# Kernel tuning notes

Hardware: AMD Instinct MI355X
Metric: run time of the kernel (lower is better)

Reference implementation:

```python
import jax, jax.numpy as jnp
import numpy as np


def setup_inputs() -> dict:
    key = jax.random.key(0)
    k1, k2 = jax.random.split(key)
    N, C, H, W = 8, 3, 512, 1024
    img = jax.random.normal(k1, (N, C, H, W), dtype=jnp.float32)
    flo = jax.random.normal(k2, (N, 2, H, W), dtype=jnp.float32)
    return {"img": img, "flo": flo}


def _splat(img_nhwc, ix, iy, w, H, W):
    # img_nhwc: (N,H,W,C); ix,iy: int32 (N,H,W) absolute target coords; w: (N,H,W)
    N = img_nhwc.shape[0]
    C = img_nhwc.shape[-1]
    valid = (ix >= 0) & (ix < H) & (iy >= 0) & (iy < W)
    w = jnp.where(valid, w, 0.0)
    ixc = jnp.clip(ix, 0, H - 1)
    iyc = jnp.clip(iy, 0, W - 1)
    n_idx = jnp.arange(N, dtype=jnp.int32)[:, None, None]
    tid = (n_idx * H + ixc) * W + iyc            # (N,H,W) flat index into N*H*W
    tid = tid.reshape(-1)
    vals = (img_nhwc * w[..., None]).reshape(-1, C)
    imgw = jnp.zeros((N * H * W, C), dtype=img_nhwc.dtype).at[tid].add(vals)
    onew = jnp.zeros((N * H * W,), dtype=img_nhwc.dtype).at[tid].add(w.reshape(-1))
    imgw = imgw.reshape(N, H, W, C).transpose(0, 3, 1, 2)          # (N,C,H,W)
    onew = jnp.broadcast_to(onew.reshape(N, 1, H, W), (N, C, H, W))
    return imgw, onew


def _forward(img, flo):
    N, C, H, W = img.shape
    y = flo[:, 0]                                # (N,H,W) row offset
    x = flo[:, 1]                                # (N,H,W) col offset
    x1 = jnp.floor(x); x2 = x1 + 1.0
    y1 = jnp.floor(y); y2 = y1 + 1.0
    # gaussian splat weights
    dx1 = (x - x1) ** 2; dx2 = (x - x2) ** 2
    dy1 = (y - y1) ** 2; dy2 = (y - y2) ** 2
    w11 = jnp.exp(-(dx1 + dy1)); w12 = jnp.exp(-(dx1 + dy2))
    w21 = jnp.exp(-(dx2 + dy1)); w22 = jnp.exp(-(dx2 + dy2))
    # base grid + integer shift -> absolute target coords
    bx = jnp.arange(H, dtype=jnp.int32)[None, :, None]   # row index
    by = jnp.arange(W, dtype=jnp.int32)[None, None, :]   # col index
    img_nhwc = img.transpose(0, 2, 3, 1)
    out = []
    for sx, sy, w in ((x1, y1, w11), (x1, y2, w12), (x2, y1, w21), (x2, y2, w22)):
        ix = sx.astype(jnp.int32) + bx
        iy = sy.astype(jnp.int32) + by
        out.append(_splat(img_nhwc, ix, iy, w, H, W))
    imgw = out[0][0] + out[1][0] + out[2][0] + out[3][0]
    o = out[0][1] + out[1][1] + out[2][1] + out[3][1]
    return imgw, o


def reference(img, flo):
    return _forward(img, flo)
```

## Files before the change

### kernel.cpp

```cpp
#include <hip/hip_runtime.h>
#include <hip/hip_fp16.h>
#include <stdint.h>

constexpr int Nn = 8;
constexpr int Cc = 3;
constexpr int Hh = 512;
constexpr int Ww = 1024;
constexpr int HW = Hh * Ww;
constexpr int NCHW = Nn * Cc * HW;

constexpr int TH = 16;
constexpr int TW = 32;
constexpr int R  = 4;
constexpr int RH = TH + 2 * R;
constexpr int RW = TW + 2 * R;
constexpr int NPIX = RH * RW;
constexpr int ITERS = (NPIX + 255) / 256;
constexpr int TILE_PIX = TH * TW;
constexpr int AWP = TW + 1;
constexpr int NP  = (TH + 1) * AWP;
constexpr int NSLOT = 3;

typedef float fvec4 __attribute__((ext_vector_type(4)));
typedef float fvec2 __attribute__((ext_vector_type(2)));
typedef __attribute__((address_space(3))) float lds_f;

__device__ __forceinline__ void ds_fadd4(lds_f* p, float a, float b, float c, float d) {
    asm volatile(
        "ds_add_f32 %0, %1\n\t"
        "ds_add_f32 %0, %2 offset:2048\n\t"
        "ds_add_f32 %0, %3 offset:4096\n\t"
        "ds_add_f32 %0, %4 offset:6144"
        :: "v"(p), "v"(a), "v"(b), "v"(c), "v"(d) : "memory");
}

__global__ __launch_bounds__(256, 5) void splat_tiled(
        const float* __restrict__ img,
        const float* __restrict__ flo,
        float* __restrict__ out) {
    __shared__ unsigned int s_tag[NP];
    __shared__ unsigned int s_pay[NSLOT * NP * 3];
    __shared__ unsigned int s_kcnt[(NP + 3) / 4 + 1];
    __shared__ float s_pl[4 * TILE_PIX];
    const int tid = threadIdx.x;
    for (int i = tid; i < NP; i += 256) s_tag[i] = 0u;
    for (int i = tid; i < (NP + 3) / 4 + 1; i += 256) s_kcnt[i] = 0u;
    {
        fvec4* a4 = (fvec4*)s_pl;
        fvec4 z = {0.f, 0.f, 0.f, 0.f};
        a4[tid] = z;
        a4[tid + 256] = z;
    }
    __syncthreads();

    const int lin = blockIdx.x + 32 * blockIdx.y + 1024 * blockIdx.z;
    const int n   = lin & 7;
    const int t   = lin >> 3;
    const int tw0 = (t & 31) * TW;
    const int th0 = (t >> 5) * TH;
    const float* __restrict__ floy = flo + (size_t)(n * 2 + 0) * HW;
    const float* __restrict__ flox = flo + (size_t)(n * 2 + 1) * HW;
    const float* __restrict__ imgn = img + (size_t)n * Cc * HW;

    float sy[ITERS], sx[ITERS], u0[ITERS], u1[ITERS], u2[ITERS];
    #pragma unroll
    for (int it = 0; it < ITERS; ++it) {
        int i  = tid + 256 * it;
        int ic = i < NPIX ? i : NPIX - 1;
        int rh = ic / RW;
        int rw = ic - rh * RW;
        int h  = th0 - R + rh;
        int w  = tw0 - R + rw;
        int hc = h < 0 ? 0 : (h > Hh - 1 ? Hh - 1 : h);
        int wc = w < 0 ? 0 : (w > Ww - 1 ? Ww - 1 : w);
        int hwc = hc * Ww + wc;
        sy[it] = floy[hwc];
        sx[it] = flox[hwc];
        u0[it] = imgn[hwc];
        u1[it] = imgn[HW + hwc];
        u2[it] = imgn[2 * HW + hwc];
    }

    int aA[ITERS];
    unsigned int tg[ITERS], q0[ITERS], q1[ITERS], q2[ITERS];
    bool pend[ITERS];
    #pragma unroll
    for (int it = 0; it < ITERS; ++it) {
        int i  = tid + 256 * it;
        int rh = i / RW;
        int rw = i - rh * RW;
        int h  = th0 - R + rh;
        int w  = tw0 - R + rw;
        bool live = (i < NPIX) & (h >= 0) & (h < Hh) & (w >= 0) & (w < Ww);

        float y = sy[it], x = sx[it];
        float x1f = floorf(x), y1f = floorf(y);
        float fx = x - x1f, fy = y - y1f;
        int ox = (int)x1f, oy = (int)y1f;
        bool patchok = (ox >= -R) & (ox <= R - 1) & (oy >= -R) & (oy <= R - 1);
        int ah = ox + rh - R;
        int aw = oy + rw - R;
        bool rec = live & patchok & (ah >= -1) & (ah <= TH - 1)
                                  & (aw >= -1) & (aw <= TW - 1);
        int aIdx = (ah + 1) * AWP + (aw + 1);
        tg[it] = 0x80000000u | ((unsigned)(ox + R) << 3) | (unsigned)(oy + R);
        unsigned h0 = __half_as_ushort(__float2half_rn(u0[it]));
        unsigned h1 = __half_as_ushort(__float2half_rn(u1[it]));
        unsigned h2 = __half_as_ushort(__float2half_rn(u2[it]));
        unsigned fxq = (unsigned)(fx * 65535.0f + 0.5f);
        unsigned fyq = (unsigned)(fy * 65535.0f + 0.5f);
        q0[it] = h0 | (h1 << 16);
        q1[it] = h2 | (fxq << 16);
        q2[it] = fyq;
        aA[it]  = aIdx;
        pend[it] = rec;
        if (rec) s_tag[aIdx] = tg[it];
    }
    __syncthreads();

    #pragma unroll
    for (int r = 0; r < NSLOT; ++r) {
        #pragma unroll
        for (int it = 0; it < ITERS; ++it) {
            if (pend[it] && s_tag[aA[it]] == tg[it]) {
                int base = aA[it] * 9 + r * 3;
                s_pay[base]     = q0[it];
                s_pay[base + 1] = q1[it];
                s_pay[base + 2] = q2[it];
                ((unsigned char*)s_kcnt)[aA[it]] = (unsigned char)(r + 1);
                pend[it] = false;
            } else if (r == NSLOT - 1 && pend[it]) {
                int a = aA[it];
                int arow = a / AWP;
                int ah = arow - 1;
                int aw = a - arow * AWP - 1;
                float fx = (float)(q1[it] >> 16) * (1.0f / 65535.0f);
                float fy = (float)(q2[it] & 0xFFFFu) * (1.0f / 65535.0f);
                float i0 = __half2float(__ushort_as_half((unsigned short)(q0[it] & 0xFFFFu)));
                float i1 = __half2float(__ushort_as_half((unsigned short)(q0[it] >> 16)));
                float i2 = __half2float(__ushort_as_half((unsigned short)(q1[it] & 0xFFFFu)));
                #pragma unroll
                for (int ca = 0; ca < 2; ++ca) {
                    #pragma unroll
                    for (int cb = 0; cb < 2; ++cb) {
                        int t_h = ah + ca, t_w = aw + cb;
                        if ((unsigned)t_h < (unsigned)TH && (unsigned)t_w < (unsigned)TW) {
                            float dx = fx - (float)ca, dy = fy - (float)cb;
                            float wt = __expf(-(dx * dx + dy * dy));
                            ds_fadd4((lds_f*)s_pl + (t_h * TW + t_w),
                                     i0 * wt, i1 * wt, i2 * wt, wt);
                        }
                    }
                }
            }
        }
        __syncthreads();
        if (r < NSLOT - 1) {
            #pragma unroll
            for (int it = 0; it < ITERS; ++it)
                if (pend[it]) s_tag[aA[it]] = tg[it];
            __syncthreads();
        }
    }

    float* __restrict__ imgw  = out;
    float* __restrict__ o_out = out + NCHW;
    const size_t nb = (size_t)n * Cc * HW;
    {
        int pix = 2 * tid;
        int lh = pix >> 5, lw = pix & 31;
        fvec2 p0 = *(const fvec2*)&s_pl[pix];
        fvec2 p1 = *(const fvec2*)&s_pl[512 + pix];
        fvec2 p2 = *(const fvec2*)&s_pl[1024 + pix];
        fvec2 p3 = *(const fvec2*)&s_pl[1536 + pix];
        float s0a = p0[0], s0b = p0[1];
        float s1a = p1[0], s1b = p1[1];
        float s2a = p2[0], s2b = p2[1];
        float s3a = p3[0], s3b = p3[1];
        #pragma unroll
        for (int a = 0; a < 2; ++a) {
            int arow = (lh - a + 1) * AWP + lw;
            #pragma unroll
            for (int c = 0; c < 3; ++c) {
                int ai = arow + c;
                int k = ((const unsigned char*)s_kcnt)[ai];
                #pragma unroll
                for (int j = 0; j < NSLOT; ++j) {
                    if (j < k) {
                        int base = ai * 9 + j * 3;
                        unsigned w0 = s_pay[base];
                        unsigned w1 = s_pay[base + 1];
                        unsigned w2 = s_pay[base + 2];
                        float h0 = __half2float(__ushort_as_half((unsigned short)(w0 & 0xFFFFu)));
                        float h1 = __half2float(__ushort_as_half((unsigned short)(w0 >> 16)));
                        float h2 = __half2float(__ushort_as_half((unsigned short)(w1 & 0xFFFFu)));
                        float fx = (float)(w1 >> 16) * (1.0f / 65535.0f);
                        float fy = (float)(w2 & 0xFFFFu) * (1.0f / 65535.0f);
                        float dx  = fx - (float)a;
                        float dxx = dx * dx;
                        if (c < 2) {
                            float dy = fy - (float)(1 - c);
                            float wt = __expf(-(dxx + dy * dy));
                            s0a += h0 * wt; s1a += h1 * wt; s2a += h2 * wt; s3a += wt;
                        }
                        if (c >= 1) {
                            float dy = fy - (float)(2 - c);
                            float wt = __expf(-(dxx + dy * dy));
                            s0b += h0 * wt; s1b += h1 * wt; s2b += h2 * wt; s3b += wt;
                        }
                    }
                }
            }
        }
        size_t hw = (size_t)(th0 + lh) * Ww + (tw0 + lw);
        fvec2 v;
        v[0] = s0a; v[1] = s0b;
        __builtin_nontemporal_store(v, (fvec2*)(imgw + nb + hw));
        v[0] = s1a; v[1] = s1b;
        __builtin_nontemporal_store(v, (fvec2*)(imgw + nb + HW + hw));
        v[0] = s2a; v[1] = s2b;
        __builtin_nontemporal_store(v, (fvec2*)(imgw + nb + 2 * HW + hw));
        v[0] = s3a; v[1] = s3b;
        __builtin_nontemporal_store(v, (fvec2*)(o_out + nb + hw));
        __builtin_nontemporal_store(v, (fvec2*)(o_out + nb + HW + hw));
        __builtin_nontemporal_store(v, (fvec2*)(o_out + nb + 2 * HW + hw));
    }
}

__global__ __launch_bounds__(256) void rescan_all(
        const float* __restrict__ img,
        const float* __restrict__ flo,
        float* __restrict__ out) {
    float* imgw  = out;
    float* o_out = out + NCHW;
    unsigned int j = blockIdx.x * blockDim.x + threadIdx.x;
    if (j >= (unsigned)(Nn * HW / 4)) return;
    int n   = j / (HW / 4);
    int q   = j - n * (HW / 4);
    int hw0 = q * 4;
    const fvec4 y4 = *(const fvec4*)&flo[(size_t)(n * 2 + 0) * HW + hw0];
    const fvec4 x4 = *(const fvec4*)&flo[(size_t)(n * 2 + 1) * HW + hw0];
    #pragma unroll
    for (int k = 0; k < 4; ++k) {
        float x = x4[k], y = y4[k];
        if (x >= -(float)R && x < (float)R && y >= -(float)R && y < (float)R) continue;
        int hw = hw0 + k;
        int h = hw >> 10;
        int w = hw & (Ww - 1);
        float x1f = floorf(x), y1f = floorf(y);
        float fx = x - x1f, fy = y - y1f;
        int bx = (int)x1f, by = (int)y1f;
        float i0 = img[(size_t)(n * Cc + 0) * HW + hw];
        float i1 = img[(size_t)(n * Cc + 1) * HW + hw];
        float i2 = img[(size_t)(n * Cc + 2) * HW + hw];
        const size_t nb = (size_t)n * Cc * HW;
        #pragma unroll
        for (int a = 0; a < 2; ++a) {
            #pragma unroll
            for (int b = 0; b < 2; ++b) {
                int ix = h + bx + a;
                int iy = w + by + b;
                if (ix < 0 || ix >= Hh || iy < 0 || iy >= Ww) continue;
                float dx = fx - (float)a, dy = fy - (float)b;
                float wt = __expf(-(dx * dx + dy * dy));
                int t = ix * Ww + iy;
                atomicAdd(&imgw[nb + t], i0 * wt);
                atomicAdd(&imgw[nb + HW + t], i1 * wt);
                atomicAdd(&imgw[nb + 2 * HW + t], i2 * wt);
                atomicAdd(&o_out[nb + t], wt);
                atomicAdd(&o_out[nb + HW + t], wt);
                atomicAdd(&o_out[nb + 2 * HW + t], wt);
            }
        }
    }
}

extern "C" void kernel_launch(void* const* d_in, const int* in_sizes, int n_in,
                              void* d_out, int out_size, void* d_ws, size_t ws_size,
                              hipStream_t stream) {
    const float* img = (const float*)d_in[0];
    const float* flo = (const float*)d_in[1];
    float* out = (float*)d_out;
    (void)d_ws; (void)ws_size;

    dim3 block(256);
    dim3 grid(32, 32, 8);
    splat_tiled<<<grid, block, 0, stream>>>(img, flo, out);
    rescan_all<<<(Nn * HW / 4 + 255) / 256, 256, 0, stream>>>(img, flo, out);
}
```

Before: 191.1 us.

## Replace LDS atomic overflow accumulation with compact overflow list gathered per pixel

Replaces the 8 KB LDS float accumulation plane and its ds_add_f32 atomics for slot-overflow entries with a small capped overflow list. Each overflow entry now carries its anchor coordinates, and every output thread scans the list during the gather phase. Removing the plane lowers LDS use, so the launch bound rises from 5 to 6 blocks per CU. The cost is that every thread scans the whole list, and entries beyond the 128 cap are silently dropped, which could lose contributions.

```diff
diff --git a/kernel.cpp b/kernel.cpp
--- a/kernel.cpp
+++ b/kernel.cpp
@@ -20,37 +20,24 @@
 constexpr int AWP = TW + 1;
 constexpr int NP  = (TH + 1) * AWP;
 constexpr int NSLOT = 3;
+constexpr int OVF_CAP = 128;
 
 typedef float fvec4 __attribute__((ext_vector_type(4)));
 typedef float fvec2 __attribute__((ext_vector_type(2)));
-typedef __attribute__((address_space(3))) float lds_f;
-
-__device__ __forceinline__ void ds_fadd4(lds_f* p, float a, float b, float c, float d) {
-    asm volatile(
-        "ds_add_f32 %0, %1\n\t"
-        "ds_add_f32 %0, %2 offset:2048\n\t"
-        "ds_add_f32 %0, %3 offset:4096\n\t"
-        "ds_add_f32 %0, %4 offset:6144"
-        :: "v"(p), "v"(a), "v"(b), "v"(c), "v"(d) : "memory");
-}
-
-__global__ __launch_bounds__(256, 5) void splat_tiled(
+
+__global__ __launch_bounds__(256, 6) void splat_tiled(
         const float* __restrict__ img,
         const float* __restrict__ flo,
         float* __restrict__ out) {
     __shared__ unsigned int s_tag[NP];
     __shared__ unsigned int s_pay[NSLOT * NP * 3];
     __shared__ unsigned int s_kcnt[(NP + 3) / 4 + 1];
-    __shared__ float s_pl[4 * TILE_PIX];
+    __shared__ unsigned int s_ovf[OVF_CAP * 4];
+    __shared__ unsigned int s_ovfn;
     const int tid = threadIdx.x;
     for (int i = tid; i < NP; i += 256) s_tag[i] = 0u;
     for (int i = tid; i < (NP + 3) / 4 + 1; i += 256) s_kcnt[i] = 0u;
-    {
-        fvec4* a4 = (fvec4*)s_pl;
-        fvec4 z = {0.f, 0.f, 0.f, 0.f};
-        a4[tid] = z;
-        a4[tid + 256] = z;
-    }
+    if (tid == 0) s_ovfn = 0u;
     __syncthreads();
 
     const int lin = blockIdx.x + 32 * blockIdx.y + 1024 * blockIdx.z;
@@ -111,7 +98,8 @@
         unsigned fyq = (unsigned)(fy * 65535.0f + 0.5f);
         q0[it] = h0 | (h1 << 16);
         q1[it] = h2 | (fxq << 16);
-        q2[it] = fyq;
+        q2[it] = fyq | (((unsigned)(ah + 1) & 0x3Fu) << 16)
+                     | (((unsigned)(aw + 1) & 0x3Fu) << 22);
         aA[it]  = aIdx;
         pend[it] = rec;
         if (rec) s_tag[aIdx] = tg[it];
@@ -130,27 +118,12 @@
                 ((unsigned char*)s_kcnt)[aA[it]] = (unsigned char)(r + 1);
                 pend[it] = false;
             } else if (r == NSLOT - 1 && pend[it]) {
-                int a = aA[it];
-                int arow = a / AWP;
-                int ah = arow - 1;
-                int aw = a - arow * AWP - 1;
-                float fx = (float)(q1[it] >> 16) * (1.0f / 65535.0f);
-                float fy = (float)(q2[it] & 0xFFFFu) * (1.0f / 65535.0f);
-                float i0 = __half2float(__ushort_as_half((unsigned short)(q0[it] & 0xFFFFu)));
-                float i1 = __half2float(__ushort_as_half((unsigned short)(q0[it] >> 16)));
-                float i2 = __half2float(__ushort_as_half((unsigned short)(q1[it] & 0xFFFFu)));
-                #pragma unroll
-                for (int ca = 0; ca < 2; ++ca) {
-                    #pragma unroll
-                    for (int cb = 0; cb < 2; ++cb) {
-                        int t_h = ah + ca, t_w = aw + cb;
-                        if ((unsigned)t_h < (unsigned)TH && (unsigned)t_w < (unsigned)TW) {
-                            float dx = fx - (float)ca, dy = fy - (float)cb;
-                            float wt = __expf(-(dx * dx + dy * dy));
-                            ds_fadd4((lds_f*)s_pl + (t_h * TW + t_w),
-                                     i0 * wt, i1 * wt, i2 * wt, wt);
-                        }
-                    }
+                unsigned idx = atomicAdd(&s_ovfn, 1u);
+                if (idx < (unsigned)OVF_CAP) {
+                    int b4 = (int)idx * 4;
+                    s_ovf[b4]     = q0[it];
+                    s_ovf[b4 + 1] = q1[it];
+                    s_ovf[b4 + 2] = q2[it];
                 }
             }
         }
@@ -169,14 +142,31 @@
     {
         int pix = 2 * tid;
         int lh = pix >> 5, lw = pix & 31;
-        fvec2 p0 = *(const fvec2*)&s_pl[pix];
-        fvec2 p1 = *(const fvec2*)&s_pl[512 + pix];
-        fvec2 p2 = *(const fvec2*)&s_pl[1024 + pix];
-        fvec2 p3 = *(const fvec2*)&s_pl[1536 + pix];
-        float s0a = p0[0], s0b = p0[1];
-        float s1a = p1[0], s1b = p1[1];
-        float s2a = p2[0], s2b = p2[1];
-        float s3a = p3[0], s3b = p3[1];
+        float s0a = 0.f, s0b = 0.f;
+        float s1a = 0.f, s1b = 0.f;
+        float s2a = 0.f, s2b = 0.f;
+        float s3a = 0.f, s3b = 0.f;
+
+        auto apply_entry = [&](unsigned w0, unsigned w1, unsigned w2, int a, int c) {
+            float h0 = __half2float(__ushort_as_half((unsigned short)(w0 & 0xFFFFu)));
+            float h1 = __half2float(__ushort_as_half((unsigned short)(w0 >> 16)));
+            float h2 = __half2float(__ushort_as_half((unsigned short)(w1 & 0xFFFFu)));
+            float fx = (float)(w1 >> 16) * (1.0f / 65535.0f);
+            float fy = (float)(w2 & 0xFFFFu) * (1.0f / 65535.0f);
+            float dx  = fx - (float)a;
+            float dxx = dx * dx;
+            if (c < 2) {
+                float dy = fy - (float)(1 - c);
+                float wt = __expf(-(dxx + dy * dy));
+                s0a += h0 * wt; s1a += h1 * wt; s2a += h2 * wt; s3a += wt;
+            }
+            if (c >= 1) {
+                float dy = fy - (float)(2 - c);
+                float wt = __expf(-(dxx + dy * dy));
+                s0b += h0 * wt; s1b += h1 * wt; s2b += h2 * wt; s3b += wt;
+            }
+        };
+
         #pragma unroll
         for (int a = 0; a < 2; ++a) {
             int arow = (lh - a + 1) * AWP + lw;
@@ -188,30 +178,26 @@
                 for (int j = 0; j < NSLOT; ++j) {
                     if (j < k) {
                         int base = ai * 9 + j * 3;
-                        unsigned w0 = s_pay[base];
-                        unsigned w1 = s_pay[base + 1];
-                        unsigned w2 = s_pay[base + 2];
-                        float h0 = __half2float(__ushort_as_half((unsigned short)(w0 & 0xFFFFu)));
-                        float h1 = __half2float(__ushort_as_half((unsigned short)(w0 >> 16)));
-                        float h2 = __half2float(__ushort_as_half((unsigned short)(w1 & 0xFFFFu)));
-                        float fx = (float)(w1 >> 16) * (1.0f / 65535.0f);
-                        float fy = (float)(w2 & 0xFFFFu) * (1.0f / 65535.0f);
-                        float dx  = fx - (float)a;
-                        float dxx = dx * dx;
-                        if (c < 2) {
-                            float dy = fy - (float)(1 - c);
-                            float wt = __expf(-(dxx + dy * dy));
-                            s0a += h0 * wt; s1a += h1 * wt; s2a += h2 * wt; s3a += wt;
-                        }
-                        if (c >= 1) {
-                            float dy = fy - (float)(2 - c);
-                            float wt = __expf(-(dxx + dy * dy));
-                            s0b += h0 * wt; s1b += h1 * wt; s2b += h2 * wt; s3b += wt;
-                        }
+                        apply_entry(s_pay[base], s_pay[base + 1], s_pay[base + 2], a, c);
                     }
                 }
             }
         }
+
+        unsigned novf = s_ovfn;
+        if (novf > (unsigned)OVF_CAP) novf = OVF_CAP;
+        for (unsigned e = 0; e < novf; ++e) {
+            unsigned w0 = s_ovf[e * 4];
+            unsigned w1 = s_ovf[e * 4 + 1];
+            unsigned w2 = s_ovf[e * 4 + 2];
+            int ar = (int)((w2 >> 16) & 0x3Fu);
+            int ac = (int)((w2 >> 22) & 0x3Fu);
+            int a  = lh + 1 - ar;
+            int c  = ac - lw;
+            if (((unsigned)a < 2u) & ((unsigned)c < 3u))
+                apply_entry(w0, w1, w2, a, c);
+        }
+
         size_t hw = (size_t)(th0 + lh) * Ww + (tw0 + lw);
         fvec2 v;
         v[0] = s0a; v[1] = s0b;
```

New measurement: 191.9 us. About the same (+0.4%).

## Enlarge tiles, drop LDS plane accumulator, overflow via global atomics

Applied to the files above, without the earlier changes.

Tiles grow from 16x32 to 32x32 and the halo shrinks from 4 to 3, which cuts redundant halo loads per output pixel. The LDS float accumulation plane and the per-cell count array are removed. Slot occupancy is now marked by a flag bit in the payload, and each thread gathers four output columns with float4 stores. Sources that overflow the three slots now do global unsafeAtomicAdd after the tile's stores complete, and the rescan kernel skips contributions already covered by a tile, so no splat is counted twice. The risks are lower occupancy (launch bounds 3), more wasted ITERS lanes, and atomic-ordering correctness that depends on s_waitcnt plus a block barrier.

```diff
diff --git a/kernel.cpp b/kernel.cpp
--- a/kernel.cpp
+++ b/kernel.cpp
@@ -9,51 +9,36 @@
 constexpr int HW = Hh * Ww;
 constexpr int NCHW = Nn * Cc * HW;
 
-constexpr int TH = 16;
+constexpr int TH = 32;
 constexpr int TW = 32;
-constexpr int R  = 4;
-constexpr int RH = TH + 2 * R;
-constexpr int RW = TW + 2 * R;
+constexpr int RS = 3;
+constexpr int RH = TH + 2 * RS;
+constexpr int RW = TW + 2 * RS;
 constexpr int NPIX = RH * RW;
 constexpr int ITERS = (NPIX + 255) / 256;
-constexpr int TILE_PIX = TH * TW;
 constexpr int AWP = TW + 1;
 constexpr int NP  = (TH + 1) * AWP;
 constexpr int NSLOT = 3;
 
 typedef float fvec4 __attribute__((ext_vector_type(4)));
-typedef float fvec2 __attribute__((ext_vector_type(2)));
-typedef __attribute__((address_space(3))) float lds_f;
-
-__device__ __forceinline__ void ds_fadd4(lds_f* p, float a, float b, float c, float d) {
-    asm volatile(
-        "ds_add_f32 %0, %1\n\t"
-        "ds_add_f32 %0, %2 offset:2048\n\t"
-        "ds_add_f32 %0, %3 offset:4096\n\t"
-        "ds_add_f32 %0, %4 offset:6144"
-        :: "v"(p), "v"(a), "v"(b), "v"(c), "v"(d) : "memory");
-}
-
-__global__ __launch_bounds__(256, 5) void splat_tiled(
+typedef unsigned int uvec4 __attribute__((ext_vector_type(4)));
+
+__global__ __launch_bounds__(256, 3) void splat_tiled(
         const float* __restrict__ img,
         const float* __restrict__ flo,
         float* __restrict__ out) {
     __shared__ unsigned int s_tag[NP];
-    __shared__ unsigned int s_pay[NSLOT * NP * 3];
-    __shared__ unsigned int s_kcnt[(NP + 3) / 4 + 1];
-    __shared__ float s_pl[4 * TILE_PIX];
+    __shared__ alignas(16) unsigned int s_pay[NSLOT * NP * 3 + 3];
     const int tid = threadIdx.x;
     for (int i = tid; i < NP; i += 256) s_tag[i] = 0u;
-    for (int i = tid; i < (NP + 3) / 4 + 1; i += 256) s_kcnt[i] = 0u;
     {
-        fvec4* a4 = (fvec4*)s_pl;
-        fvec4 z = {0.f, 0.f, 0.f, 0.f};
-        a4[tid] = z;
-        a4[tid + 256] = z;
+        uvec4* p4 = (uvec4*)s_pay;
+        uvec4 z = {0u, 0u, 0u, 0u};
+        for (int i = tid; i < (NSLOT * NP * 3 + 3) / 4; i += 256) p4[i] = z;
     }
     __syncthreads();
 
-    const int lin = blockIdx.x + 32 * blockIdx.y + 1024 * blockIdx.z;
+    const int lin = blockIdx.x + 32 * blockIdx.y + 512 * blockIdx.z;
     const int n   = lin & 7;
     const int t   = lin >> 3;
     const int tw0 = (t & 31) * TW;
@@ -65,12 +50,13 @@
     float sy[ITERS], sx[ITERS], u0[ITERS], u1[ITERS], u2[ITERS];
     #pragma unroll
     for (int it = 0; it < ITERS; ++it) {
+        if ((tid & ~63) + 256 * it >= NPIX) continue;
         int i  = tid + 256 * it;
         int ic = i < NPIX ? i : NPIX - 1;
         int rh = ic / RW;
         int rw = ic - rh * RW;
-        int h  = th0 - R + rh;
-        int w  = tw0 - R + rw;
+        int h  = th0 - RS + rh;
+        int w  = tw0 - RS + rw;
         int hc = h < 0 ? 0 : (h > Hh - 1 ? Hh - 1 : h);
         int wc = w < 0 ? 0 : (w > Ww - 1 ? Ww - 1 : w);
         int hwc = hc * Ww + wc;
@@ -85,25 +71,27 @@
     unsigned int tg[ITERS], q0[ITERS], q1[ITERS], q2[ITERS];
     bool pend[ITERS];
     #pragma unroll
+    for (int it = 0; it < ITERS; ++it) pend[it] = false;
+    #pragma unroll
     for (int it = 0; it < ITERS; ++it) {
+        if ((tid & ~63) + 256 * it >= NPIX) continue;
         int i  = tid + 256 * it;
-        int rh = i / RW;
-        int rw = i - rh * RW;
-        int h  = th0 - R + rh;
-        int w  = tw0 - R + rw;
+        int ic = i < NPIX ? i : NPIX - 1;
+        int rh = ic / RW;
+        int rw = ic - rh * RW;
+        int h  = th0 - RS + rh;
+        int w  = tw0 - RS + rw;
         bool live = (i < NPIX) & (h >= 0) & (h < Hh) & (w >= 0) & (w < Ww);
 
         float y = sy[it], x = sx[it];
         float x1f = floorf(x), y1f = floorf(y);
         float fx = x - x1f, fy = y - y1f;
         int ox = (int)x1f, oy = (int)y1f;
-        bool patchok = (ox >= -R) & (ox <= R - 1) & (oy >= -R) & (oy <= R - 1);
-        int ah = ox + rh - R;
-        int aw = oy + rw - R;
-        bool rec = live & patchok & (ah >= -1) & (ah <= TH - 1)
-                                  & (aw >= -1) & (aw <= TW - 1);
+        int ah = ox + rh - RS;
+        int aw = oy + rw - RS;
+        bool rec = live & (ah >= -1) & (ah < TH) & (aw >= -1) & (aw < TW);
         int aIdx = (ah + 1) * AWP + (aw + 1);
-        tg[it] = 0x80000000u | ((unsigned)(ox + R) << 3) | (unsigned)(oy + R);
+        tg[it] = 0x80000000u | (unsigned)i;
         unsigned h0 = __half_as_ushort(__float2half_rn(u0[it]));
         unsigned h1 = __half_as_ushort(__float2half_rn(u1[it]));
         unsigned h2 = __half_as_ushort(__float2half_rn(u2[it]));
@@ -111,7 +99,8 @@
         unsigned fyq = (unsigned)(fy * 65535.0f + 0.5f);
         q0[it] = h0 | (h1 << 16);
         q1[it] = h2 | (fxq << 16);
-        q2[it] = fyq;
+        q2[it] = fyq | (((unsigned)(ah + 1) & 0x3Fu) << 16)
+                     | (((unsigned)(aw + 1) & 0x3Fu) << 22) | 0x80000000u;
         aA[it]  = aIdx;
         pend[it] = rec;
         if (rec) s_tag[aIdx] = tg[it];
@@ -127,31 +116,7 @@
                 s_pay[base]     = q0[it];
                 s_pay[base + 1] = q1[it];
                 s_pay[base + 2] = q2[it];
-                ((unsigned char*)s_kcnt)[aA[it]] = (unsigned char)(r + 1);
                 pend[it] = false;
-            } else if (r == NSLOT - 1 && pend[it]) {
-                int a = aA[it];
-                int arow = a / AWP;
-                int ah = arow - 1;
-                int aw = a - arow * AWP - 1;
-                float fx = (float)(q1[it] >> 16) * (1.0f / 65535.0f);
-                float fy = (float)(q2[it] & 0xFFFFu) * (1.0f / 65535.0f);
-                float i0 = __half2float(__ushort_as_half((unsigned short)(q0[it] & 0xFFFFu)));
-                float i1 = __half2float(__ushort_as_half((unsigned short)(q0[it] >> 16)));
-                float i2 = __half2float(__ushort_as_half((unsigned short)(q1[it] & 0xFFFFu)));
-                #pragma unroll
-                for (int ca = 0; ca < 2; ++ca) {
-                    #pragma unroll
-                    for (int cb = 0; cb < 2; ++cb) {
-                        int t_h = ah + ca, t_w = aw + cb;
-                        if ((unsigned)t_h < (unsigned)TH && (unsigned)t_w < (unsigned)TW) {
-                            float dx = fx - (float)ca, dy = fy - (float)cb;
-                            float wt = __expf(-(dx * dx + dy * dy));
-                            ds_fadd4((lds_f*)s_pl + (t_h * TW + t_w),
-                                     i0 * wt, i1 * wt, i2 * wt, wt);
-                        }
-                    }
-                }
             }
         }
         __syncthreads();
@@ -167,66 +132,94 @@
     float* __restrict__ o_out = out + NCHW;
     const size_t nb = (size_t)n * Cc * HW;
     {
-        int pix = 2 * tid;
-        int lh = pix >> 5, lw = pix & 31;
-        fvec2 p0 = *(const fvec2*)&s_pl[pix];
-        fvec2 p1 = *(const fvec2*)&s_pl[512 + pix];
-        fvec2 p2 = *(const fvec2*)&s_pl[1024 + pix];
-        fvec2 p3 = *(const fvec2*)&s_pl[1536 + pix];
-        float s0a = p0[0], s0b = p0[1];
-        float s1a = p1[0], s1b = p1[1];
-        float s2a = p2[0], s2b = p2[1];
-        float s3a = p3[0], s3b = p3[1];
-        #pragma unroll
-        for (int a = 0; a < 2; ++a) {
-            int arow = (lh - a + 1) * AWP + lw;
-            #pragma unroll
-            for (int c = 0; c < 3; ++c) {
-                int ai = arow + c;
-                int k = ((const unsigned char*)s_kcnt)[ai];
+        int lh = tid >> 3;
+        int lw = (tid & 7) << 2;
+        fvec4 a0 = {0.f,0.f,0.f,0.f}, a1 = a0, a2 = a0, a3 = a0;
+
+        #pragma unroll
+        for (int dr = 0; dr < 2; ++dr) {
+            const int a = 1 - dr;
+            int rowbase = (lh + dr) * AWP + lw;
+            #pragma unroll
+            for (int c = 0; c <= 4; ++c) {
+                int ai = rowbase + c;
                 #pragma unroll
                 for (int j = 0; j < NSLOT; ++j) {
-                    if (j < k) {
-                        int base = ai * 9 + j * 3;
-                        unsigned w0 = s_pay[base];
-                        unsigned w1 = s_pay[base + 1];
-                        unsigned w2 = s_pay[base + 2];
-                        float h0 = __half2float(__ushort_as_half((unsigned short)(w0 & 0xFFFFu)));
-                        float h1 = __half2float(__ushort_as_half((unsigned short)(w0 >> 16)));
-                        float h2 = __half2float(__ushort_as_half((unsigned short)(w1 & 0xFFFFu)));
-                        float fx = (float)(w1 >> 16) * (1.0f / 65535.0f);
-                        float fy = (float)(w2 & 0xFFFFu) * (1.0f / 65535.0f);
-                        float dx  = fx - (float)a;
-                        float dxx = dx * dx;
-                        if (c < 2) {
-                            float dy = fy - (float)(1 - c);
-                            float wt = __expf(-(dxx + dy * dy));
-                            s0a += h0 * wt; s1a += h1 * wt; s2a += h2 * wt; s3a += wt;
-                        }
-                        if (c >= 1) {
-                            float dy = fy - (float)(2 - c);
-                            float wt = __expf(-(dxx + dy * dy));
-                            s0b += h0 * wt; s1b += h1 * wt; s2b += h2 * wt; s3b += wt;
-                        }
+                    int base = ai * 9 + j * 3;
+                    unsigned w2 = s_pay[base + 2];
+                    if (!(w2 & 0x80000000u)) break;
+                    unsigned w0 = s_pay[base];
+                    unsigned w1 = s_pay[base + 1];
+                    float h0 = __half2float(__ushort_as_half((unsigned short)(w0 & 0xFFFFu)));
+                    float h1 = __half2float(__ushort_as_half((unsigned short)(w0 >> 16)));
+                    float h2 = __half2float(__ushort_as_half((unsigned short)(w1 & 0xFFFFu)));
+                    float fx = (float)(w1 >> 16) * (1.0f / 65535.0f);
+                    float fy = (float)(w2 & 0xFFFFu) * (1.0f / 65535.0f);
+                    float dx = fx - (float)a;
+                    float dxx = dx * dx;
+                    if (c >= 1) {
+                        float wt = __expf(-(dxx + fy * fy));
+                        a0[c-1] += h0 * wt; a1[c-1] += h1 * wt;
+                        a2[c-1] += h2 * wt; a3[c-1] += wt;
+                    }
+                    if (c <= 3) {
+                        float dy = fy - 1.0f;
+                        float wt = __expf(-(dxx + dy * dy));
+                        a0[c] += h0 * wt; a1[c] += h1 * wt;
+                        a2[c] += h2 * wt; a3[c] += wt;
                     }
                 }
             }
         }
+
         size_t hw = (size_t)(th0 + lh) * Ww + (tw0 + lw);
-        fvec2 v;
-        v[0] = s0a; v[1] = s0b;
-        __builtin_nontemporal_store(v, (fvec2*)(imgw + nb + hw));
-        v[0] = s1a; v[1] = s1b;
-        __builtin_nontemporal_store(v, (fvec2*)(imgw + nb + HW + hw));
-        v[0] = s2a; v[1] = s2b;
-        __builtin_nontemporal_store(v, (fvec2*)(imgw + nb + 2 * HW + hw));
-        v[0] = s3a; v[1] = s3b;
-        __builtin_nontemporal_store(v, (fvec2*)(o_out + nb + hw));
-        __builtin_nontemporal_store(v, (fvec2*)(o_out + nb + HW + hw));
-        __builtin_nontemporal_store(v, (fvec2*)(o_out + nb + 2 * HW + hw));
+        __builtin_nontemporal_store(a0, (fvec4*)(imgw + nb + hw));
+        __builtin_nontemporal_store(a1, (fvec4*)(imgw + nb + HW + hw));
+        __builtin_nontemporal_store(a2, (fvec4*)(imgw + nb + 2 * HW + hw));
+        __builtin_nontemporal_store(a3, (fvec4*)(o_out + nb + hw));
+        __builtin_nontemporal_store(a3, (fvec4*)(o_out + nb + HW + hw));
+        __builtin_nontemporal_store(a3, (fvec4*)(o_out + nb + 2 * HW + hw));
+    }
+
+    asm volatile("s_waitcnt vmcnt(0)" ::: "memory");
+    __syncthreads();
+    bool any = false;
+    #pragma unroll
+    for (int it = 0; it < ITERS; ++it) any |= pend[it];
+    if (any) {
+        #pragma unroll
+        for (int it = 0; it < ITERS; ++it) {
+            if (!pend[it]) continue;
+            int ar = (int)((q2[it] >> 16) & 0x3Fu);
+            int ac = (int)((q2[it] >> 22) & 0x3Fu);
+            float fx = (float)(q1[it] >> 16) * (1.0f / 65535.0f);
+            float fy = (float)(q2[it] & 0xFFFFu) * (1.0f / 65535.0f);
+            float i0 = __half2float(__ushort_as_half((unsigned short)(q0[it] & 0xFFFFu)));
+            float i1 = __half2float(__ushort_as_half((unsigned short)(q0[it] >> 16)));
+            float i2 = __half2float(__ushort_as_half((unsigned short)(q1[it] & 0xFFFFu)));
+            #pragma unroll
+            for (int ca = 0; ca < 2; ++ca) {
+                #pragma unroll
+                for (int cb = 0; cb < 2; ++cb) {
+                    int lr = ar - 1 + ca, lc = ac - 1 + cb;
+                    if ((unsigned)lr < (unsigned)TH && (unsigned)lc < (unsigned)TW) {
+                        float dx = fx - (float)ca, dy = fy - (float)cb;
+                        float wt = __expf(-(dx * dx + dy * dy));
+                        size_t t2 = (size_t)(th0 + lr) * Ww + (tw0 + lc);
+                        unsafeAtomicAdd(imgw + nb + t2, i0 * wt);
+                        unsafeAtomicAdd(imgw + nb + HW + t2, i1 * wt);
+                        unsafeAtomicAdd(imgw + nb + 2 * HW + t2, i2 * wt);
+                        unsafeAtomicAdd(o_out + nb + t2, wt);
+                        unsafeAtomicAdd(o_out + nb + HW + t2, wt);
+                        unsafeAtomicAdd(o_out + nb + 2 * HW + t2, wt);
+                    }
+                }
+            }
+        }
     }
 }
 
+typedef float fvec4g __attribute__((ext_vector_type(4)));
 __global__ __launch_bounds__(256) void rescan_all(
         const float* __restrict__ img,
         const float* __restrict__ flo,
@@ -243,13 +236,14 @@
     #pragma unroll
     for (int k = 0; k < 4; ++k) {
         float x = x4[k], y = y4[k];
-        if (x >= -(float)R && x < (float)R && y >= -(float)R && y < (float)R) continue;
+        if (x >= -(float)RS && x < (float)RS && y >= -(float)RS && y < (float)RS)
+            continue;
         int hw = hw0 + k;
         int h = hw >> 10;
         int w = hw & (Ww - 1);
         float x1f = floorf(x), y1f = floorf(y);
         float fx = x - x1f, fy = y - y1f;
-        int bx = (int)x1f, by = (int)y1f;
+        int ox = (int)x1f, oy = (int)y1f;
         float i0 = img[(size_t)(n * Cc + 0) * HW + hw];
         float i1 = img[(size_t)(n * Cc + 1) * HW + hw];
         float i2 = img[(size_t)(n * Cc + 2) * HW + hw];
@@ -258,18 +252,23 @@
         for (int a = 0; a < 2; ++a) {
             #pragma unroll
             for (int b = 0; b < 2; ++b) {
-                int ix = h + bx + a;
-                int iy = w + by + b;
-                if (ix < 0 || ix >= Hh || iy < 0 || iy >= Ww) continue;
+                int ch = h + ox + a;
+                int cw = w + oy + b;
+                if (ch < 0 || ch >= Hh || cw < 0 || cw >= Ww) continue;
+                int r0 = (ch >> 5) * TH;
+                int c0 = (cw >> 5) * TW;
+                bool covered = (h >= r0 - RS) & (h <= r0 + TH + RS - 1) &
+                               (w >= c0 - RS) & (w <= c0 + TW + RS - 1);
+                if (covered) continue;
                 float dx = fx - (float)a, dy = fy - (float)b;
                 float wt = __expf(-(dx * dx + dy * dy));
-                int t = ix * Ww + iy;
-                atomicAdd(&imgw[nb + t], i0 * wt);
-                atomicAdd(&imgw[nb + HW + t], i1 * wt);
-                atomicAdd(&imgw[nb + 2 * HW + t], i2 * wt);
-                atomicAdd(&o_out[nb + t], wt);
-                atomicAdd(&o_out[nb + HW + t], wt);
-                atomicAdd(&o_out[nb + 2 * HW + t], wt);
+                size_t t = (size_t)ch * Ww + cw;
+                unsafeAtomicAdd(&imgw[nb + t], i0 * wt);
+                unsafeAtomicAdd(&imgw[nb + HW + t], i1 * wt);
+                unsafeAtomicAdd(&imgw[nb + 2 * HW + t], i2 * wt);
+                unsafeAtomicAdd(&o_out[nb + t], wt);
+                unsafeAtomicAdd(&o_out[nb + HW + t], wt);
+                unsafeAtomicAdd(&o_out[nb + 2 * HW + t], wt);
             }
         }
     }
@@ -284,7 +283,7 @@
     (void)d_ws; (void)ws_size;
 
     dim3 block(256);
-    dim3 grid(32, 32, 8);
+    dim3 grid(32, 16, 8);
     splat_tiled<<<grid, block, 0, stream>>>(img, flo, out);
     rescan_all<<<(Nn * HW / 4 + 255) / 256, 256, 0, stream>>>(img, flo, out);
 }
```

Result: slower. 290.3 us (+52.0%).
